# Kernel tuning notes

Hardware: AMD Instinct MI355X
Metric: run time of the kernel (lower is better)

Reference implementation:

```python
import jax, jax.numpy as jnp
import numpy as np

M0, M1, H = 128, 64, 8            # scalar mul, vector mul, num heads
AH0, AH1 = 16, 8                  # per-head irreps: 16x0e + 8x1e
D = M0 + 3 * M1                   # 320 node feature dim
DTP0 = M0 + M1                    # 192 scalar channels out of depthwise TP
DTP1 = M0 + 2 * M1                # 256 vector channels out of depthwise TP
WNUM = 2 * M0 + 3 * M1            # 448 TP path weights (uvu, edge mul=1)
RAD_IN, RAD_HID = 32, 64
N_NODES, N_EDGES = 10000, 160000
INV_SQRT3 = 1.0 / np.sqrt(3.0)    # CG norm for 1e x 1e -> 0e
INV_SQRT2 = 1.0 / np.sqrt(2.0)    # CG norm for 1e x 1e -> 1e


def _split(x, m0, m1):
    # e3nn layout: [m0 scalars | m1 vectors * 3 components]
    return x[..., :m0], x[..., m0:].reshape(x.shape[:-1] + (m1, 3))


def _silu(x):
    return x * jax.nn.sigmoid(x)


def _smooth_leaky(x, a=0.2):
    # SmoothLeakyReLU from equiformer
    return 0.5 * (1 + a) * x + 0.5 * (1 - a) * x * (2.0 * jax.nn.sigmoid(x) - 1.0)


def _dtp(s, v, e0, e1, w):
    # depthwise (uvu) tensor product of (M0x0e + M1x1e) with edge attr (1x0e + 1x1e)
    # s [E,M0], v [E,M1,3], e0 [E,1], e1 [E,3], w [E,WNUM] or [WNUM] (internal)
    w1, w2, w3, w4, w5 = jnp.split(w, [M0, 2 * M0, 2 * M0 + M1, 2 * M0 + 2 * M1], axis=-1)
    os1 = w1 * s * e0                                                  # 0e x 0e -> 0e
    os2 = w4 * (jnp.einsum('emc,ec->em', v, e1) * INV_SQRT3)           # 1e x 1e -> 0e
    ov1 = (w2 * s)[..., None] * e1[:, None, :]                         # 0e x 1e -> 1e
    ov2 = w3[..., None] * v * e0[..., None]                            # 1e x 0e -> 1e
    ov3 = w5[..., None] * (jnp.cross(v, e1[:, None, :]) * INV_SQRT2)   # 1e x 1e -> 1e
    return jnp.concatenate([os1, os2], -1), jnp.concatenate([ov1, ov2, ov3], -2)


def _forward(node_input, edge_src, edge_dst, edge_attr, edge_scalars,
             Wsrc_s, Wsrc_v, bsrc, Wdst_s, Wdst_v,
             rad_W1, rad_b1, rad_W2, rad_off,
             Wact_s, bact, Wact_v, Walpha, balpha, w_int,
             Wval_s, bval, Wval_v, alpha_dot, Wproj_s, bproj, Wproj_v):
    N = node_input.shape[0]
    E = edge_src.shape[0]
    s, v = _split(node_input, M0, M1)
    # merge_src / merge_dst: per-irrep linear (bias only on scalars of src)
    ms_s = s @ Wsrc_s + bsrc
    ms_v = jnp.einsum('nmc,mk->nkc', v, Wsrc_v)
    md_s = s @ Wdst_s
    md_v = jnp.einsum('nmc,mk->nkc', v, Wdst_v)
    msg_s = ms_s[edge_src] + md_s[edge_dst]          # [E, M0]
    msg_v = ms_v[edge_src] + md_v[edge_dst]          # [E, M1, 3]
    e0, e1 = edge_attr[:, :1], edge_attr[:, 1:4]
    # radial profile MLP -> edge-dependent TP weights
    w = _silu(edge_scalars @ rad_W1 + rad_b1) @ rad_W2 + rad_off       # [E, WNUM]
    ds, dv = _dtp(msg_s, msg_v, e0, e1, w)           # [E, DTP0], [E, DTP1, 3]
    # alpha branch: linear on TP scalars -> heads -> smooth leaky -> dot
    al = _smooth_leaky((ds @ Walpha + balpha).reshape(E, H, AH0))
    logits = jnp.einsum('ehk,hk->eh', al, alpha_dot[0])                # [E, H]
    # value branch: sep_act.lin + gate
    scal = ds @ Wact_s + bact                        # [E, M0+M1] scalars+gates
    gated_v = jnp.einsum('emc,mk->ekc', dv, Wact_v)  # [E, M1, 3]
    val_s = _silu(scal[:, :M0])
    val_v = gated_v * jax.nn.sigmoid(scal[:, M0:])[..., None]
    # sep_value: depthwise TP with internal weights + linear
    vs, vv = _dtp(val_s, val_v, e0, e1, w_int)
    out_s = vs @ Wval_s + bval                       # [E, H*AH0]
    out_v = jnp.einsum('emc,mk->ekc', vv, Wval_v)    # [E, H*AH1, 3]
    value = jnp.concatenate([out_s.reshape(E, H, AH0),
                             out_v.reshape(E, H, AH1 * 3)], axis=2)    # [E, H, 40]
    # softmax over incoming edges per destination node
    mx = jax.lax.stop_gradient(jax.ops.segment_max(logits, edge_dst, num_segments=N))
    mx = jnp.where(jnp.isfinite(mx), mx, 0.0)
    ex = jnp.exp(logits - mx[edge_dst])
    den = jax.ops.segment_sum(ex, edge_dst, num_segments=N)
    alpha = ex / (den[edge_dst] + 1e-16)             # [E, H]
    agg = jax.ops.segment_sum(value * alpha[..., None], edge_dst, num_segments=N)
    # heads2vec + output projection
    node_s = agg[:, :, :AH0].reshape(N, H * AH0)
    node_v = agg[:, :, AH0:].reshape(N, H * AH1, 3)
    po_s = node_s @ Wproj_s + bproj
    po_v = jnp.einsum('nmc,mk->nkc', node_v, Wproj_v)
    return jnp.concatenate([po_s, po_v.reshape(N, M1 * 3)], axis=1)


def _lin(key, fi, fo):
    return jax.random.normal(key, (fi, fo), jnp.float32) / np.sqrt(fi)


def setup_inputs() -> dict:
    ks = iter(jax.random.split(jax.random.key(0), 40))
    inp = {}
    inp['node_input'] = jax.random.normal(next(ks), (N_NODES, D), jnp.float32)
    inp['edge_src'] = jax.random.randint(next(ks), (N_EDGES,), 0, N_NODES)
    inp['edge_dst'] = jax.random.randint(next(ks), (N_EDGES,), 0, N_NODES)
    inp['edge_attr'] = jax.random.normal(next(ks), (N_EDGES, 4), jnp.float32)
    inp['edge_scalars'] = jax.random.normal(next(ks), (N_EDGES, RAD_IN), jnp.float32)
    inp['Wsrc_s'] = _lin(next(ks), M0, M0)
    inp['Wsrc_v'] = _lin(next(ks), M1, M1)
    inp['bsrc'] = 0.1 * jax.random.normal(next(ks), (M0,), jnp.float32)
    inp['Wdst_s'] = _lin(next(ks), M0, M0)
    inp['Wdst_v'] = _lin(next(ks), M1, M1)
    inp['rad_W1'] = _lin(next(ks), RAD_IN, RAD_HID)
    inp['rad_b1'] = 0.1 * jax.random.normal(next(ks), (RAD_HID,), jnp.float32)
    inp['rad_W2'] = _lin(next(ks), RAD_HID, WNUM)
    inp['rad_off'] = 0.1 * jax.random.normal(next(ks), (WNUM,), jnp.float32)
    inp['Wact_s'] = _lin(next(ks), DTP0, M0 + M1)
    inp['bact'] = 0.1 * jax.random.normal(next(ks), (M0 + M1,), jnp.float32)
    inp['Wact_v'] = _lin(next(ks), DTP1, M1)
    inp['Walpha'] = _lin(next(ks), DTP0, H * AH0)
    inp['balpha'] = 0.1 * jax.random.normal(next(ks), (H * AH0,), jnp.float32)
    inp['w_int'] = jax.random.normal(next(ks), (WNUM,), jnp.float32)
    inp['Wval_s'] = _lin(next(ks), DTP0, H * AH0)
    inp['bval'] = 0.1 * jax.random.normal(next(ks), (H * AH0,), jnp.float32)
    inp['Wval_v'] = _lin(next(ks), DTP1, H * AH1)
    inp['alpha_dot'] = jax.random.normal(next(ks), (1, H, AH0), jnp.float32) / np.sqrt(AH0)
    inp['Wproj_s'] = _lin(next(ks), H * AH0, M0)
    inp['bproj'] = 0.1 * jax.random.normal(next(ks), (M0,), jnp.float32)
    inp['Wproj_v'] = _lin(next(ks), H * AH1, M1)
    return inp


def reference(node_input, edge_src, edge_dst, edge_attr, edge_scalars,
              Wsrc_s, Wsrc_v, bsrc, Wdst_s, Wdst_v,
              rad_W1, rad_b1, rad_W2, rad_off,
              Wact_s, bact, Wact_v, Walpha, balpha, w_int,
              Wval_s, bval, Wval_v, alpha_dot, Wproj_s, bproj, Wproj_v):
    return _forward(node_input, edge_src, edge_dst, edge_attr, edge_scalars,
                    Wsrc_s, Wsrc_v, bsrc, Wdst_s, Wdst_v,
                    rad_W1, rad_b1, rad_W2, rad_off,
                    Wact_s, bact, Wact_v, Walpha, balpha, w_int,
                    Wval_s, bval, Wval_v, alpha_dot, Wproj_s, bproj, Wproj_v)
```

## Files before the change

kernel.cpp:

```cpp
#include <hip/hip_runtime.h>

#define NN 10000
#define NE 160000
#define INV_SQRT3f 0.57735026918962576f
#define INV_SQRT2f 0.70710678118654752f
#define VPLU 640000

typedef short bshort8 __attribute__((ext_vector_type(8)));
typedef float floatx4 __attribute__((ext_vector_type(4)));
#define MFMA16(a,b,c) __builtin_amdgcn_mfma_f32_16x16x32_bf16((a),(b),(c),0,0,0)

__device__ __forceinline__ float sigm(float x){ return 1.f/(1.f+__expf(-x)); }
__device__ __forceinline__ float siluf(float x){ return x*sigm(x); }
__device__ __forceinline__ float sleaky(float x){ return 0.6f*x + 0.4f*x*(2.f*sigm(x)-1.f); }
__device__ __forceinline__ unsigned short f2bf(float f){
  return (unsigned short)((__float_as_uint(f) + 0x8000u)>>16);
}
__device__ __forceinline__ float bf2f(unsigned short h){
  return __uint_as_float(((unsigned)h)<<16);
}
__device__ __forceinline__ unsigned cvtpk(float lo, float hi){
  unsigned r;
  asm("v_cvt_pk_bf16_f32 %0, %1, %2" : "=v"(r) : "v"(lo), "v"(hi));
  return r;
}
__device__ __forceinline__ float lo16f(unsigned u){ return __uint_as_float(u<<16); }
__device__ __forceinline__ float hi16f(unsigned u){ return __uint_as_float(u & 0xffff0000u); }

#define O_W1   0
#define O_W2   2048
#define O_WAS  30720
#define O_WAVT 67584
#define O_WAVB 75776
#define O_WVS  83968
#define O_WVVT 108544
#define O_WVVB 116736
#define O_WALP 124928
#define SWZ_TOTAL 149504

__global__ __launch_bounds__(256) void k_init(float* __restrict__ num,
                                              float* __restrict__ den,
                                              int* __restrict__ cnt) {
  int i = blockIdx.x*256 + threadIdx.x;
  if (i < NN*320) num[i] = 0.f;
  if (i < NN*8) den[i] = 0.f;
  if (i < NN) cnt[i] = 0;
}

__global__ __launch_bounds__(256) void k_hist(const int* __restrict__ edst,
                                              int* __restrict__ cnt) {
  int e = blockIdx.x*256 + threadIdx.x;
  if (e < NE) atomicAdd(&cnt[edst[e]], 1);
}

__global__ __launch_bounds__(256) void k_scan(const int* __restrict__ cnt,
                                              int* __restrict__ offs) {
  __shared__ int wsum[4];
  const int tid = threadIdx.x;
  const int lane = tid & 63, wave = tid >> 6;
  int v[40]; int s = 0;
  #pragma unroll
  for (int j=0;j<40;j++){ int i = tid*40+j; v[j] = (i<NN)?cnt[i]:0; s += v[j]; }
  int incl = s;
  #pragma unroll
  for (int d=1; d<64; d<<=1) { int t = __shfl_up(incl, d, 64); if (lane>=d) incl += t; }
  if (lane==63) wsum[wave] = incl;
  __syncthreads();
  int wbase = 0;
  for (int w=0; w<wave; ++w) wbase += wsum[w];
  int excl = wbase + incl - s;
  #pragma unroll
  for (int j=0;j<40;j++){ int i = tid*40+j; if (i<NN) offs[i] = excl; excl += v[j]; }
}

__global__ __launch_bounds__(256) void k_scatter(const int* __restrict__ edst,
                                                 int* __restrict__ offs,
                                                 int* __restrict__ perm) {
  int e = blockIdx.x*256 + threadIdx.x;
  if (e < NE) {
    int pos = atomicAdd(&offs[edst[e]], 1);
    perm[pos] = e;
  }
}

__global__ __launch_bounds__(256) void node_pre(
    const float* __restrict__ x,
    const float* __restrict__ Wsrc_s, const float* __restrict__ Wsrc_v,
    const float* __restrict__ bsrc,
    const float* __restrict__ Wdst_s, const float* __restrict__ Wdst_v,
    unsigned short* __restrict__ ms_s, unsigned short* __restrict__ md_s,
    unsigned short* __restrict__ ms_v, unsigned short* __restrict__ md_v) {
  __shared__ __align__(16) float s_s[128*8];
  __shared__ __align__(16) float s_v[192*8];
  const int tid = threadIdx.x;
  const int n0 = blockIdx.x*8;
  for (int idx = tid; idx < 8*320; idx += 256) {
    int n = idx/320, d = idx - n*320;
    float val = x[(n0+n)*320 + d];
    if (d < 128) s_s[d*8+n] = val;
    else         s_v[(d-128)*8+n] = val;
  }
  __syncthreads();
  {
    int g = tid>>7, j = tid&127;
    float accs[4], accd[4];
    float b = bsrc[j];
    #pragma unroll
    for (int i=0;i<4;i++){ accs[i]=b; accd[i]=0.f; }
    for (int k=0;k<128;k++) {
      float w1 = Wsrc_s[k*128+j], w2 = Wdst_s[k*128+j];
      float4 sv = *(const float4*)&s_s[k*8+g*4];
      accs[0]+=sv.x*w1; accs[1]+=sv.y*w1; accs[2]+=sv.z*w1; accs[3]+=sv.w*w1;
      accd[0]+=sv.x*w2; accd[1]+=sv.y*w2; accd[2]+=sv.z*w2; accd[3]+=sv.w*w2;
    }
    #pragma unroll
    for (int i=0;i<4;i++){ int n=n0+g*4+i; ms_s[n*128+j]=f2bf(accs[i]); md_s[n*128+j]=f2bf(accd[i]); }
  }
  if (tid < 192) {
    int c = tid>>6, k = tid&63;
    float accs[8], accd[8];
    #pragma unroll
    for (int e=0;e<8;e++){ accs[e]=0.f; accd[e]=0.f; }
    for (int m=0;m<64;m++) {
      float w1 = Wsrc_v[m*64+k], w2 = Wdst_v[m*64+k];
      float4 v0 = *(const float4*)&s_v[(m*3+c)*8];
      float4 v1 = *(const float4*)&s_v[(m*3+c)*8+4];
      accs[0]+=v0.x*w1; accs[1]+=v0.y*w1; accs[2]+=v0.z*w1; accs[3]+=v0.w*w1;
      accs[4]+=v1.x*w1; accs[5]+=v1.y*w1; accs[6]+=v1.z*w1; accs[7]+=v1.w*w1;
      accd[0]+=v0.x*w2; accd[1]+=v0.y*w2; accd[2]+=v0.z*w2; accd[3]+=v0.w*w2;
      accd[4]+=v1.x*w2; accd[5]+=v1.y*w2; accd[6]+=v1.z*w2; accd[7]+=v1.w*w2;
    }
    #pragma unroll
    for (int e=0;e<8;e++){
      int n=n0+e;
      ms_v[c*VPLU + n*64 + k] = f2bf(accs[e]);
      md_v[c*VPLU + n*64 + k] = f2bf(accd[e]);
    }
  }
}

__global__ __launch_bounds__(256) void k_prep(
    const float* __restrict__ W1, const float* __restrict__ W2,
    const float* __restrict__ WAs, const float* __restrict__ WAv,
    const float* __restrict__ WVs, const float* __restrict__ WVv,
    const float* __restrict__ WAl,
    unsigned short* __restrict__ swz) {
  int s = blockIdx.x*256 + threadIdx.x;
  if (s >= SWZ_TOTAL) return;
  const float* src; int base, N, KT, rowOff;
  if      (s < 2048)  { base=O_W1;   src=W1;  N=64;  KT=1; rowOff=0; }
  else if (s < 30720) { base=O_W2;   src=W2;  N=448; KT=2; rowOff=0; }
  else if (s < 67584) { base=O_WAS;  src=WAs; N=192; KT=6; rowOff=0; }
  else if (s < 75776) { base=O_WAVT; src=WAv; N=64;  KT=4; rowOff=0; }
  else if (s < 83968) { base=O_WAVB; src=WAv; N=64;  KT=4; rowOff=128; }
  else if (s < 108544){ base=O_WVS;  src=WVs; N=128; KT=6; rowOff=0; }
  else if (s < 116736){ base=O_WVVT; src=WVv; N=64;  KT=4; rowOff=0; }
  else if (s < 124928){ base=O_WVVB; src=WVv; N=64;  KT=4; rowOff=128; }
  else                { base=O_WALP; src=WAl; N=128; KT=6; rowOff=0; }
  int loc = s - base;
  int j = loc & 7, l = (loc>>3)&63, kt = (loc>>9)%KT, nt = loc/(512*KT);
  int row = kt*32 + (l>>4)*8 + j + rowOff;
  int col = nt*16 + (l&15);
  swz[s] = f2bf(src[row*N + col]);
}

__global__ __launch_bounds__(256, 5) void e_all(
    const unsigned short* __restrict__ ms_s, const unsigned short* __restrict__ md_s,
    const unsigned short* __restrict__ ms_v, const unsigned short* __restrict__ md_v,
    const int* __restrict__ esrc, const int* __restrict__ edst,
    const int* __restrict__ perm,
    const float* __restrict__ eattr, const float* __restrict__ escal,
    const float* __restrict__ rad_b1, const float* __restrict__ rad_off,
    const float* __restrict__ bact, const float* __restrict__ w_int,
    const float* __restrict__ bval,
    const float* __restrict__ balpha, const float* __restrict__ alpha_dot,
    const unsigned short* __restrict__ swz,
    float* __restrict__ den, float* __restrict__ num) {
  __shared__ __align__(16) char smem[30912];
  unsigned short* sw_v = (unsigned short*)smem;
  float* vout          = (float*)smem;
  unsigned short* ads  = (unsigned short*)(smem+6144);
  unsigned short* at1  = (unsigned short*)(smem+12544);
  unsigned short* advb = (unsigned short*)(smem+16896);
  unsigned short* aes  = (unsigned short*)(smem+16896);
  unsigned short* ah   = (unsigned short*)(smem+19456);
  float* s_e0 = (float*)(smem+29952);
  float* s_e1 = (float*)(smem+30016);
  float* s_ex = (float*)(smem+30208);
  int* s_eid  = (int*)(smem+30720);
  int* s_src  = (int*)(smem+30784);
  int* s_dst  = (int*)(smem+30848);
  const int tid  = threadIdx.x;
  const int lane = tid & 63, wave = tid >> 6;
  const int quad = lane >> 4, l15 = lane & 15;
  const int bswz = (blockIdx.x & 7)*1250 + (blockIdx.x >> 3);
  const int eb = bswz*16;

  if (tid < 16) {
    int eid = perm[eb+tid];
    s_eid[tid] = eid; s_src[tid] = esrc[eid]; s_dst[tid] = edst[eid];
  }
  __syncthreads();
  if (tid >= 64 && tid < 128) {
    int t = tid-64, e = t>>2, q = t&3;
    float a = eattr[s_eid[e]*4+q];
    if (q == 0) s_e0[e] = a; else s_e1[(q-1)*16+e] = a;
  }
  {
    int e = tid>>4, i0 = (tid&15)*2;
    float2 es = *(const float2*)&escal[s_eid[e]*32+i0];
    *(unsigned*)&aes[e*40+i0] = cvtpk(es.x, es.y);
  }
  __syncthreads();

  {
    int nt = wave, col = nt*16 + l15;
    bshort8 a = *(const bshort8*)&aes[l15*40 + quad*8];
    bshort8 b = *(const bshort8*)&swz[O_W1 + (nt*64 + lane)*8];
    float bb = rad_b1[col];
    floatx4 acc = {bb,bb,bb,bb};
    acc = MFMA16(a, b, acc);
    #pragma unroll
    for (int r=0;r<4;r++) ah[(quad*4+r)*72 + col] = f2bf(siluf(acc[r]));
  }
  __syncthreads();

  {
    bshort8 ha0 = *(const bshort8*)&ah[l15*72 + quad*8];
    bshort8 ha1 = *(const bshort8*)&ah[l15*72 + 32 + quad*8];
    int src_[4], dst_[4];
    #pragma unroll
    for (int r=0;r<4;r++){ int e=quad*4+r; src_[r]=s_src[e]; dst_[r]=s_dst[e]; }
    #pragma unroll
    for (int p=0;p<2;p++) {
      int nt1 = wave*2+p, nt2 = nt1+8;
      int m = nt1*16 + l15;
      float o1 = rad_off[m], o2 = rad_off[128+m];
      floatx4 a1 = {o1,o1,o1,o1}, a2 = {o2,o2,o2,o2};
      a1 = MFMA16(ha0, *(const bshort8*)&swz[O_W2 + ((nt1*2+0)*64+lane)*8], a1);
      a1 = MFMA16(ha1, *(const bshort8*)&swz[O_W2 + ((nt1*2+1)*64+lane)*8], a1);
      a2 = MFMA16(ha0, *(const bshort8*)&swz[O_W2 + ((nt2*2+0)*64+lane)*8], a2);
      a2 = MFMA16(ha1, *(const bshort8*)&swz[O_W2 + ((nt2*2+1)*64+lane)*8], a2);
      #pragma unroll
      for (int r=0;r<4;r++) {
        int e = quad*4+r;
        float msgs = bf2f(ms_s[src_[r]*128+m]) + bf2f(md_s[dst_[r]*128+m]);
        ads[e*200+m] = f2bf(a1[r]*msgs*s_e0[e]);
        at1[e*136+m] = f2bf(a2[r]*msgs);
      }
    }
    #pragma unroll
    for (int q=0;q<3;q++) {
      int nt = 16 + wave*3 + q, col = nt*16 + l15;
      float o = rad_off[col];
      floatx4 acc = {o,o,o,o};
      acc = MFMA16(ha0, *(const bshort8*)&swz[O_W2 + ((nt*2+0)*64+lane)*8], acc);
      acc = MFMA16(ha1, *(const bshort8*)&swz[O_W2 + ((nt*2+1)*64+lane)*8], acc);
      #pragma unroll
      for (int r=0;r<4;r++) sw_v[(quad*4+r)*192 + (col-256)] = f2bf(acc[r]);
    }
  }
  __syncthreads();

  #pragma unroll
  for (int it = 0; it < 2; ++it) {
    int t = tid + it*256;
    int e = t>>5, pr = t&31;
    int k0 = pr*2;
    int sb = s_src[e]*64 + k0, db = s_dst[e]*64 + k0;
    unsigned usx = *(const unsigned*)&ms_v[0*VPLU+sb];
    unsigned usy = *(const unsigned*)&ms_v[1*VPLU+sb];
    unsigned usz = *(const unsigned*)&ms_v[2*VPLU+sb];
    unsigned udx = *(const unsigned*)&md_v[0*VPLU+db];
    unsigned udy = *(const unsigned*)&md_v[1*VPLU+db];
    unsigned udz = *(const unsigned*)&md_v[2*VPLU+db];
    unsigned uw3 = *(const unsigned*)&sw_v[e*192 + k0];
    unsigned uw4 = *(const unsigned*)&sw_v[e*192 + 64 + k0];
    unsigned uw5 = *(const unsigned*)&sw_v[e*192 + 128 + k0];
    float ex1 = s_e1[0+e], ey1 = s_e1[16+e], ez1 = s_e1[32+e];
    float e0 = s_e0[e];
    float vx0 = lo16f(usx)+lo16f(udx), vx1 = hi16f(usx)+hi16f(udx);
    float vy0 = lo16f(usy)+lo16f(udy), vy1 = hi16f(usy)+hi16f(udy);
    float vz0 = lo16f(usz)+lo16f(udz), vz1 = hi16f(usz)+hi16f(udz);
    float d0 = vx0*ex1 + vy0*ey1 + vz0*ez1;
    float d1 = vx1*ex1 + vy1*ey1 + vz1*ez1;
    *(unsigned*)&ads[e*200+128+k0] =
        cvtpk(lo16f(uw4)*d0*INV_SQRT3f, hi16f(uw4)*d1*INV_SQRT3f);
    float w30 = lo16f(uw3)*e0, w31 = hi16f(uw3)*e0;
    float w50 = lo16f(uw5)*INV_SQRT2f, w51 = hi16f(uw5)*INV_SQRT2f;
    *(unsigned*)&advb[0*2176 + e*136 + k0] = cvtpk(w30*vx0, w31*vx1);
    *(unsigned*)&advb[1*2176 + e*136 + k0] = cvtpk(w30*vy0, w31*vy1);
    *(unsigned*)&advb[2*2176 + e*136 + k0] = cvtpk(w30*vz0, w31*vz1);
    *(unsigned*)&advb[0*2176 + e*136 + 64+k0] =
        cvtpk(w50*(vy0*ez1 - vz0*ey1), w51*(vy1*ez1 - vz1*ey1));
    *(unsigned*)&advb[1*2176 + e*136 + 64+k0] =
        cvtpk(w50*(vz0*ex1 - vx0*ez1), w51*(vz1*ex1 - vx1*ez1));
    *(unsigned*)&advb[2*2176 + e*136 + 64+k0] =
        cvtpk(w50*(vx0*ey1 - vy0*ex1), w51*(vx1*ey1 - vy1*ex1));
  }
  __syncthreads();

  floatx4 sc0, sc1, sc2, gsa, gb0, gb1, gb2;
  {
    bshort8 fa[6];
    #pragma unroll
    for (int kt=0;kt<6;kt++) fa[kt] = *(const bshort8*)&ads[l15*200 + kt*32 + quad*8];
    #pragma unroll
    for (int t=0;t<2;t++) {
      int h = wave*2 + t;
      int col = h*16 + l15;
      float bb = balpha[col];
      floatx4 acc = {bb,bb,bb,bb};
      #pragma unroll
      for (int kt=0;kt<6;kt++)
        acc = MFMA16(fa[kt], *(const bshort8*)&swz[O_WALP + ((h*6+kt)*64+lane)*8], acc);
      float ad = alpha_dot[col];
      float exv[4];
      #pragma unroll
      for (int r=0;r<4;r++) {
        float p = sleaky(acc[r])*ad;
        p += __shfl_xor(p, 1);
        p += __shfl_xor(p, 2);
        p += __shfl_xor(p, 4);
        p += __shfl_xor(p, 8);
        float ex = __expf(p);
        exv[r] = ex;
        if (l15 == 0) s_ex[(quad*4+r)*8+h] = ex;
      }
      if (l15 == 0) {
        float racc = exv[0]; int cur = s_dst[quad*4];
        #pragma unroll
        for (int r=1;r<4;r++) {
          int d = s_dst[quad*4+r];
          if (d != cur) { atomicAdd(&den[cur*8+h], racc); racc = 0.f; cur = d; }
          racc += exv[r];
        }
        atomicAdd(&den[cur*8+h], racc);
      }
    }
    {
      float bb = bact[wave*16 + l15];
      floatx4 a0 = {bb,bb,bb,bb};
      #pragma unroll
      for (int kt=0;kt<6;kt++)
        a0 = MFMA16(fa[kt], *(const bshort8*)&swz[O_WAS + ((wave*6+kt)*64+lane)*8], a0);
      sc0 = a0;
    }
    {
      float bb = bact[(wave+4)*16 + l15];
      floatx4 a1 = {bb,bb,bb,bb};
      #pragma unroll
      for (int kt=0;kt<6;kt++)
        a1 = MFMA16(fa[kt], *(const bshort8*)&swz[O_WAS + (((wave+4)*6+kt)*64+lane)*8], a1);
      sc1 = a1;
    }
    {
      float bb = bact[(wave+8)*16 + l15];
      floatx4 a2 = {bb,bb,bb,bb};
      #pragma unroll
      for (int kt=0;kt<6;kt++)
        a2 = MFMA16(fa[kt], *(const bshort8*)&swz[O_WAS + (((wave+8)*6+kt)*64+lane)*8], a2);
      sc2 = a2;
    }
    bshort8 ft[4];
    #pragma unroll
    for (int kt=0;kt<4;kt++) ft[kt] = *(const bshort8*)&at1[l15*136 + kt*32 + quad*8];
    {
      floatx4 acc = {0.f,0.f,0.f,0.f};
      #pragma unroll
      for (int kt=0;kt<4;kt++)
        acc = MFMA16(ft[kt], *(const bshort8*)&swz[O_WAVT + ((wave*4+kt)*64+lane)*8], acc);
      gsa = acc;
    }
    #pragma unroll
    for (int c=0;c<3;c++) {
      floatx4 acc = {0.f,0.f,0.f,0.f};
      #pragma unroll
      for (int kt=0;kt<4;kt++) {
        bshort8 fb = *(const bshort8*)&advb[c*2176 + l15*136 + kt*32 + quad*8];
        acc = MFMA16(fb, *(const bshort8*)&swz[O_WAVB + ((wave*4+kt)*64+lane)*8], acc);
      }
      if (c==0) gb0 = acc; else if (c==1) gb1 = acc; else gb2 = acc;
    }
  }
  __syncthreads();

  {
    const int k = wave*16 + l15;
    #pragma unroll
    for (int r=0;r<4;r++) {
      int row = quad*4 + r;
      float e0 = s_e0[row];
      {
        float v = siluf(sc0[r]);
        ads[row*200+k] = f2bf(w_int[k]*v*e0);
        at1[row*136+k] = f2bf(w_int[128+k]*v);
      }
      {
        int m = 64+k;
        float v = siluf(sc1[r]);
        ads[row*200+m] = f2bf(w_int[m]*v*e0);
        at1[row*136+m] = f2bf(w_int[128+m]*v);
      }
      {
        float sg = sigm(sc2[r]);
        float gs = gsa[r];
        float ex1 = s_e1[0+row], ey1 = s_e1[16+row], ez1 = s_e1[32+row];
        float v0 = (gs*ex1 + gb0[r])*sg;
        float v1 = (gs*ey1 + gb1[r])*sg;
        float v2 = (gs*ez1 + gb2[r])*sg;
        float d = v0*ex1 + v1*ey1 + v2*ez1;
        ads[row*200+128+k] = f2bf(w_int[320+k]*d*INV_SQRT3f);
        float w3v = w_int[256+k]*e0;
        float w5  = w_int[384+k]*INV_SQRT2f;
        advb[0*2176 + row*136 + k] = f2bf(w3v*v0);
        advb[1*2176 + row*136 + k] = f2bf(w3v*v1);
        advb[2*2176 + row*136 + k] = f2bf(w3v*v2);
        advb[0*2176 + row*136 + 64+k] = f2bf(w5*(v1*ez1 - v2*ey1));
        advb[1*2176 + row*136 + 64+k] = f2bf(w5*(v2*ex1 - v0*ez1));
        advb[2*2176 + row*136 + 64+k] = f2bf(w5*(v0*ey1 - v1*ex1));
      }
    }
  }
  __syncthreads();

  {
    bshort8 fa[6];
    #pragma unroll
    for (int kt=0;kt<6;kt++) fa[kt] = *(const bshort8*)&ads[l15*200 + kt*32 + quad*8];
    __syncthreads();
    #pragma unroll
    for (int t=0;t<2;t++) {
      int h = wave + 4*t;
      float bb = bval[h*16 + l15];
      floatx4 acc = {bb,bb,bb,bb};
      #pragma unroll
      for (int kt=0;kt<6;kt++)
        acc = MFMA16(fa[kt], *(const bshort8*)&swz[O_WVS + ((h*6+kt)*64+lane)*8], acc);
      #pragma unroll
      for (int r=0;r<4;r++) {
        int row = quad*4 + r;
        vout[row*132 + h*16 + l15] = acc[r]*s_ex[row*8+h];
      }
    }
  }
  __syncthreads();

  if (tid < 128) {
    const int j = tid, h = j>>4, jj = j&15;
    float acc = 0.f; int cur = s_dst[0];
    #pragma unroll
    for (int e = 0; e < 16; ++e) {
      int d = s_dst[e];
      if (d != cur) { atomicAdd(&num[cur*320 + h*40 + jj], acc); acc = 0.f; cur = d; }
      acc += vout[e*132 + j];
    }
    atomicAdd(&num[cur*320 + h*40 + jj], acc);
  }
  __syncthreads();

  {
    bshort8 ft[4];
    #pragma unroll
    for (int kt=0;kt<4;kt++) ft[kt] = *(const bshort8*)&at1[l15*136 + kt*32 + quad*8];
    floatx4 vsh = {0.f,0.f,0.f,0.f};
    #pragma unroll
    for (int kt=0;kt<4;kt++)
      vsh = MFMA16(ft[kt], *(const bshort8*)&swz[O_WVVT + ((wave*4+kt)*64+lane)*8], vsh);
    const int k = wave*16 + l15;
    const int h = k>>3, q = k&7;
    #pragma unroll
    for (int c=0;c<3;c++) {
      floatx4 acc = {0.f,0.f,0.f,0.f};
      #pragma unroll
      for (int kt=0;kt<4;kt++) {
        bshort8 fb = *(const bshort8*)&advb[c*2176 + l15*136 + kt*32 + quad*8];
        acc = MFMA16(fb, *(const bshort8*)&swz[O_WVVB + ((wave*4+kt)*64+lane)*8], acc);
      }
      #pragma unroll
      for (int r=0;r<4;r++) {
        int row = quad*4 + r;
        vout[row*194 + h*24 + q*3 + c] =
            (acc[r] + s_e1[c*16+row]*vsh[r]) * s_ex[row*8+h];
      }
    }
  }
  __syncthreads();

  if (tid < 192) {
    const int jj = tid;
    const int h = jj/24, rr = jj - h*24;
    float acc = 0.f; int cur = s_dst[0];
    #pragma unroll
    for (int e = 0; e < 16; ++e) {
      int d = s_dst[e];
      if (d != cur) { atomicAdd(&num[cur*320 + h*40 + 16 + rr], acc); acc = 0.f; cur = d; }
      acc += vout[e*194 + jj];
    }
    atomicAdd(&num[cur*320 + h*40 + 16 + rr], acc);
  }
}

__global__ __launch_bounds__(256) void node_post(
    const float* __restrict__ num, const float* __restrict__ den,
    const float* __restrict__ Wproj_s, const float* __restrict__ bproj,
    const float* __restrict__ Wproj_v, float* __restrict__ out) {
  __shared__ __align__(16) float s_ns[128*8];
  __shared__ __align__(16) float s_nv[192*8];
  const int tid = threadIdx.x;
  const int n0 = blockIdx.x*8;
  for (int idx = tid; idx < 8*320; idx += 256) {
    int n = idx/320, j = idx - n*320;
    int h = j/40, r = j - h*40;
    float a = num[(n0+n)*320+j] / (den[(n0+n)*8+h] + 1e-16f);
    if (r < 16) s_ns[(h*16+r)*8+n] = a;
    else        s_nv[(h*24 + (r-16))*8+n] = a;
  }
  __syncthreads();
  {
    int g = tid>>7, j = tid&127;
    float acc[4]; float b = bproj[j];
    #pragma unroll
    for (int i=0;i<4;i++) acc[i]=b;
    for (int k=0;k<128;k++) {
      float wv = Wproj_s[k*128+j];
      float4 s4 = *(const float4*)&s_ns[k*8+g*4];
      acc[0]+=s4.x*wv; acc[1]+=s4.y*wv; acc[2]+=s4.z*wv; acc[3]+=s4.w*wv;
    }
    #pragma unroll
    for (int i=0;i<4;i++) out[(n0+g*4+i)*320 + j] = acc[i];
  }
  if (tid < 192) {
    int c = tid>>6, k = tid&63;
    float acc[8];
    #pragma unroll
    for (int e=0;e<8;e++) acc[e]=0.f;
    for (int m=0;m<64;m++) {
      float wv = Wproj_v[m*64+k];
      float4 v0 = *(const float4*)&s_nv[(m*3+c)*8];
      float4 v1 = *(const float4*)&s_nv[(m*3+c)*8+4];
      acc[0]+=v0.x*wv; acc[1]+=v0.y*wv; acc[2]+=v0.z*wv; acc[3]+=v0.w*wv;
      acc[4]+=v1.x*wv; acc[5]+=v1.y*wv; acc[6]+=v1.z*wv; acc[7]+=v1.w*wv;
    }
    #pragma unroll
    for (int e=0;e<8;e++) out[(n0+e)*320 + 128 + k*3 + c] = acc[e];
  }
}

extern "C" void kernel_launch(void* const* d_in, const int* in_sizes, int n_in,
                              void* d_out, int out_size, void* d_ws, size_t ws_size,
                              hipStream_t stream) {
  (void)in_sizes; (void)n_in; (void)out_size; (void)ws_size;
  const float* node_input = (const float*)d_in[0];
  const int*   esrc       = (const int*)d_in[1];
  const int*   edst       = (const int*)d_in[2];
  const float* eattr      = (const float*)d_in[3];
  const float* escal      = (const float*)d_in[4];
  const float* Wsrc_s     = (const float*)d_in[5];
  const float* Wsrc_v     = (const float*)d_in[6];
  const float* bsrc       = (const float*)d_in[7];
  const float* Wdst_s     = (const float*)d_in[8];
  const float* Wdst_v     = (const float*)d_in[9];
  const float* rad_W1     = (const float*)d_in[10];
  const float* rad_b1     = (const float*)d_in[11];
  const float* rad_W2     = (const float*)d_in[12];
  const float* rad_off    = (const float*)d_in[13];
  const float* Wact_s     = (const float*)d_in[14];
  const float* bact       = (const float*)d_in[15];
  const float* Wact_v     = (const float*)d_in[16];
  const float* Walpha     = (const float*)d_in[17];
  const float* balpha     = (const float*)d_in[18];
  const float* w_int      = (const float*)d_in[19];
  const float* Wval_s     = (const float*)d_in[20];
  const float* bval       = (const float*)d_in[21];
  const float* Wval_v     = (const float*)d_in[22];
  const float* alpha_dot  = (const float*)d_in[23];
  const float* Wproj_s    = (const float*)d_in[24];
  const float* bproj      = (const float*)d_in[25];
  const float* Wproj_v    = (const float*)d_in[26];
  float* out = (float*)d_out;

  char* wsb = (char*)d_ws;
  unsigned short* ms_s16 = (unsigned short*)(wsb);
  unsigned short* md_s16 = (unsigned short*)(wsb + 2560000);
  unsigned short* ms_v16 = (unsigned short*)(wsb + 5120000);
  unsigned short* md_v16 = (unsigned short*)(wsb + 8960000);
  float* den             = (float*)(wsb + 12800000);
  float* num             = (float*)(wsb + 13120000);
  unsigned short* swz    = (unsigned short*)(wsb + 25920000);
  int* cnt  = (int*)(wsb + 26220032);
  int* offs = (int*)(wsb + 26260032);
  int* perm = (int*)(wsb + 26300032);

  k_prep<<<584, 256, 0, stream>>>(rad_W1, rad_W2, Wact_s, Wact_v, Wval_s, Wval_v, Walpha, swz);
  k_init<<<12500, 256, 0, stream>>>(num, den, cnt);
  k_hist<<<625, 256, 0, stream>>>(edst, cnt);
  k_scan<<<1, 256, 0, stream>>>(cnt, offs);
  k_scatter<<<625, 256, 0, stream>>>(edst, offs, perm);
  node_pre<<<1250, 256, 0, stream>>>(node_input, Wsrc_s, Wsrc_v, bsrc, Wdst_s, Wdst_v,
                                     ms_s16, md_s16, ms_v16, md_v16);
  e_all<<<10000, 256, 0, stream>>>(ms_s16, md_s16, ms_v16, md_v16, esrc, edst, perm, eattr, escal,
                                   rad_b1, rad_off, bact, w_int, bval,
                                   balpha, alpha_dot, swz, den, num);
  node_post<<<1250, 256, 0, stream>>>(num, den, Wproj_s, bproj, Wproj_v, out);
}
```

Before: 387.3 us.

## Fold internal TP weights into value weights, merge prep kernels, shrink edge LDS

```diff
diff --git a/kernel.cpp b/kernel.cpp
--- a/kernel.cpp
+++ b/kernel.cpp
@@ -24,8 +24,6 @@
   asm("v_cvt_pk_bf16_f32 %0, %1, %2" : "=v"(r) : "v"(lo), "v"(hi));
   return r;
 }
-__device__ __forceinline__ float lo16f(unsigned u){ return __uint_as_float(u<<16); }
-__device__ __forceinline__ float hi16f(unsigned u){ return __uint_as_float(u & 0xffff0000u); }
 
 #define O_W1   0
 #define O_W2   2048
@@ -38,13 +36,99 @@
 #define O_WALP 124928
 #define SWZ_TOTAL 149504
 
-__global__ __launch_bounds__(256) void k_init(float* __restrict__ num,
-                                              float* __restrict__ den,
-                                              int* __restrict__ cnt) {
-  int i = blockIdx.x*256 + threadIdx.x;
-  if (i < NN*320) num[i] = 0.f;
-  if (i < NN*8) den[i] = 0.f;
-  if (i < NN) cnt[i] = 0;
+__global__ __launch_bounds__(256) void k_pre_all(
+    const float* __restrict__ x,
+    const float* __restrict__ Wsrc_s, const float* __restrict__ Wsrc_v,
+    const float* __restrict__ bsrc,
+    const float* __restrict__ Wdst_s, const float* __restrict__ Wdst_v,
+    unsigned short* __restrict__ ms_s, unsigned short* __restrict__ md_s,
+    unsigned short* __restrict__ ms_v, unsigned short* __restrict__ md_v,
+    const float* __restrict__ W1, const float* __restrict__ W2,
+    const float* __restrict__ WAs, const float* __restrict__ WAv,
+    const float* __restrict__ WVs, const float* __restrict__ WVv,
+    const float* __restrict__ WAl, const float* __restrict__ w_int,
+    unsigned short* __restrict__ swz,
+    float* __restrict__ num, float* __restrict__ den, int* __restrict__ cnt) {
+  __shared__ __align__(16) float s_s[128*8];
+  __shared__ __align__(16) float s_v[192*8];
+  const int tid = threadIdx.x;
+  const int b = blockIdx.x;
+  if (b >= 1834) {
+    int base = (b-1834)*256 + tid;
+    float4 z = {0.f,0.f,0.f,0.f};
+    for (int i = base; i < 800000; i += 554496) ((float4*)num)[i] = z;
+    if (base < 20000) ((float4*)den)[base] = z;
+    if (base < 10000) cnt[base] = 0;
+    return;
+  }
+  if (b >= 1250) {
+    int s = (b-1250)*256 + tid;
+    if (s >= SWZ_TOTAL) return;
+    const float* src; int base, N, KT, rowOff;
+    if      (s < 2048)  { base=O_W1;   src=W1;  N=64;  KT=1; rowOff=0; }
+    else if (s < 30720) { base=O_W2;   src=W2;  N=448; KT=2; rowOff=0; }
+    else if (s < 67584) { base=O_WAS;  src=WAs; N=192; KT=6; rowOff=0; }
+    else if (s < 75776) { base=O_WAVT; src=WAv; N=64;  KT=4; rowOff=0; }
+    else if (s < 83968) { base=O_WAVB; src=WAv; N=64;  KT=4; rowOff=128; }
+    else if (s < 108544){ base=O_WVS;  src=WVs; N=128; KT=6; rowOff=0; }
+    else if (s < 116736){ base=O_WVVT; src=WVv; N=64;  KT=4; rowOff=0; }
+    else if (s < 124928){ base=O_WVVB; src=WVv; N=64;  KT=4; rowOff=128; }
+    else                { base=O_WALP; src=WAl; N=128; KT=6; rowOff=0; }
+    int loc = s - base;
+    int j = loc & 7, l = (loc>>3)&63, kt = (loc>>9)%KT, nt = loc/(512*KT);
+    int row = kt*32 + (l>>4)*8 + j + rowOff;
+    int col = nt*16 + (l&15);
+    float scl = 1.f;
+    if      (base == O_WVS)  scl = (row < 128) ? w_int[row] : w_int[192+row]*INV_SQRT3f;
+    else if (base == O_WVVT) scl = w_int[128+row];
+    else if (base == O_WVVB) scl = (row < 192) ? w_int[128+row] : w_int[192+row]*INV_SQRT2f;
+    swz[s] = f2bf(src[row*N + col] * scl);
+    return;
+  }
+  const int n0 = b*8;
+  for (int idx = tid; idx < 8*320; idx += 256) {
+    int n = idx/320, d = idx - n*320;
+    float val = x[(n0+n)*320 + d];
+    if (d < 128) s_s[d*8+n] = val;
+    else         s_v[(d-128)*8+n] = val;
+  }
+  __syncthreads();
+  {
+    int g = tid>>7, j = tid&127;
+    float accs[4], accd[4];
+    float bb = bsrc[j];
+    #pragma unroll
+    for (int i=0;i<4;i++){ accs[i]=bb; accd[i]=0.f; }
+    for (int k=0;k<128;k++) {
+      float w1 = Wsrc_s[k*128+j], w2 = Wdst_s[k*128+j];
+      float4 sv = *(const float4*)&s_s[k*8+g*4];
+      accs[0]+=sv.x*w1; accs[1]+=sv.y*w1; accs[2]+=sv.z*w1; accs[3]+=sv.w*w1;
+      accd[0]+=sv.x*w2; accd[1]+=sv.y*w2; accd[2]+=sv.z*w2; accd[3]+=sv.w*w2;
+    }
+    #pragma unroll
+    for (int i=0;i<4;i++){ int n=n0+g*4+i; ms_s[n*128+j]=f2bf(accs[i]); md_s[n*128+j]=f2bf(accd[i]); }
+  }
+  if (tid < 192) {
+    int c = tid>>6, k = tid&63;
+    float accs[8], accd[8];
+    #pragma unroll
+    for (int e=0;e<8;e++){ accs[e]=0.f; accd[e]=0.f; }
+    for (int m=0;m<64;m++) {
+      float w1 = Wsrc_v[m*64+k], w2 = Wdst_v[m*64+k];
+      float4 v0 = *(const float4*)&s_v[(m*3+c)*8];
+      float4 v1 = *(const float4*)&s_v[(m*3+c)*8+4];
+      accs[0]+=v0.x*w1; accs[1]+=v0.y*w1; accs[2]+=v0.z*w1; accs[3]+=v0.w*w1;
+      accs[4]+=v1.x*w1; accs[5]+=v1.y*w1; accs[6]+=v1.z*w1; accs[7]+=v1.w*w1;
+      accd[0]+=v0.x*w2; accd[1]+=v0.y*w2; accd[2]+=v0.z*w2; accd[3]+=v0.w*w2;
+      accd[4]+=v1.x*w2; accd[5]+=v1.y*w2; accd[6]+=v1.z*w2; accd[7]+=v1.w*w2;
+    }
+    #pragma unroll
+    for (int e=0;e<8;e++){
+      int n=n0+e;
+      ms_v[c*VPLU + n*64 + k] = f2bf(accs[e]);
+      md_v[c*VPLU + n*64 + k] = f2bf(accd[e]);
+    }
+  }
 }
 
 __global__ __launch_bounds__(256) void k_hist(const int* __restrict__ edst,
@@ -83,113 +167,31 @@
   }
 }
 
-__global__ __launch_bounds__(256) void node_pre(
-    const float* __restrict__ x,
-    const float* __restrict__ Wsrc_s, const float* __restrict__ Wsrc_v,
-    const float* __restrict__ bsrc,
-    const float* __restrict__ Wdst_s, const float* __restrict__ Wdst_v,
-    unsigned short* __restrict__ ms_s, unsigned short* __restrict__ md_s,
-    unsigned short* __restrict__ ms_v, unsigned short* __restrict__ md_v) {
-  __shared__ __align__(16) float s_s[128*8];
-  __shared__ __align__(16) float s_v[192*8];
-  const int tid = threadIdx.x;
-  const int n0 = blockIdx.x*8;
-  for (int idx = tid; idx < 8*320; idx += 256) {
-    int n = idx/320, d = idx - n*320;
-    float val = x[(n0+n)*320 + d];
-    if (d < 128) s_s[d*8+n] = val;
-    else         s_v[(d-128)*8+n] = val;
-  }
-  __syncthreads();
-  {
-    int g = tid>>7, j = tid&127;
-    float accs[4], accd[4];
-    float b = bsrc[j];
-    #pragma unroll
-    for (int i=0;i<4;i++){ accs[i]=b; accd[i]=0.f; }
-    for (int k=0;k<128;k++) {
-      float w1 = Wsrc_s[k*128+j], w2 = Wdst_s[k*128+j];
-      float4 sv = *(const float4*)&s_s[k*8+g*4];
-      accs[0]+=sv.x*w1; accs[1]+=sv.y*w1; accs[2]+=sv.z*w1; accs[3]+=sv.w*w1;
-      accd[0]+=sv.x*w2; accd[1]+=sv.y*w2; accd[2]+=sv.z*w2; accd[3]+=sv.w*w2;
-    }
-    #pragma unroll
-    for (int i=0;i<4;i++){ int n=n0+g*4+i; ms_s[n*128+j]=f2bf(accs[i]); md_s[n*128+j]=f2bf(accd[i]); }
-  }
-  if (tid < 192) {
-    int c = tid>>6, k = tid&63;
-    float accs[8], accd[8];
-    #pragma unroll
-    for (int e=0;e<8;e++){ accs[e]=0.f; accd[e]=0.f; }
-    for (int m=0;m<64;m++) {
-      float w1 = Wsrc_v[m*64+k], w2 = Wdst_v[m*64+k];
-      float4 v0 = *(const float4*)&s_v[(m*3+c)*8];
-      float4 v1 = *(const float4*)&s_v[(m*3+c)*8+4];
-      accs[0]+=v0.x*w1; accs[1]+=v0.y*w1; accs[2]+=v0.z*w1; accs[3]+=v0.w*w1;
-      accs[4]+=v1.x*w1; accs[5]+=v1.y*w1; accs[6]+=v1.z*w1; accs[7]+=v1.w*w1;
-      accd[0]+=v0.x*w2; accd[1]+=v0.y*w2; accd[2]+=v0.z*w2; accd[3]+=v0.w*w2;
-      accd[4]+=v1.x*w2; accd[5]+=v1.y*w2; accd[6]+=v1.z*w2; accd[7]+=v1.w*w2;
-    }
-    #pragma unroll
-    for (int e=0;e<8;e++){
-      int n=n0+e;
-      ms_v[c*VPLU + n*64 + k] = f2bf(accs[e]);
-      md_v[c*VPLU + n*64 + k] = f2bf(accd[e]);
-    }
-  }
-}
-
-__global__ __launch_bounds__(256) void k_prep(
-    const float* __restrict__ W1, const float* __restrict__ W2,
-    const float* __restrict__ WAs, const float* __restrict__ WAv,
-    const float* __restrict__ WVs, const float* __restrict__ WVv,
-    const float* __restrict__ WAl,
-    unsigned short* __restrict__ swz) {
-  int s = blockIdx.x*256 + threadIdx.x;
-  if (s >= SWZ_TOTAL) return;
-  const float* src; int base, N, KT, rowOff;
-  if      (s < 2048)  { base=O_W1;   src=W1;  N=64;  KT=1; rowOff=0; }
-  else if (s < 30720) { base=O_W2;   src=W2;  N=448; KT=2; rowOff=0; }
-  else if (s < 67584) { base=O_WAS;  src=WAs; N=192; KT=6; rowOff=0; }
-  else if (s < 75776) { base=O_WAVT; src=WAv; N=64;  KT=4; rowOff=0; }
-  else if (s < 83968) { base=O_WAVB; src=WAv; N=64;  KT=4; rowOff=128; }
-  else if (s < 108544){ base=O_WVS;  src=WVs; N=128; KT=6; rowOff=0; }
-  else if (s < 116736){ base=O_WVVT; src=WVv; N=64;  KT=4; rowOff=0; }
-  else if (s < 124928){ base=O_WVVB; src=WVv; N=64;  KT=4; rowOff=128; }
-  else                { base=O_WALP; src=WAl; N=128; KT=6; rowOff=0; }
-  int loc = s - base;
-  int j = loc & 7, l = (loc>>3)&63, kt = (loc>>9)%KT, nt = loc/(512*KT);
-  int row = kt*32 + (l>>4)*8 + j + rowOff;
-  int col = nt*16 + (l&15);
-  swz[s] = f2bf(src[row*N + col]);
-}
-
-__global__ __launch_bounds__(256, 5) void e_all(
+__global__ __launch_bounds__(256, 6) void e_all(
     const unsigned short* __restrict__ ms_s, const unsigned short* __restrict__ md_s,
     const unsigned short* __restrict__ ms_v, const unsigned short* __restrict__ md_v,
     const int* __restrict__ esrc, const int* __restrict__ edst,
     const int* __restrict__ perm,
     const float* __restrict__ eattr, const float* __restrict__ escal,
     const float* __restrict__ rad_b1, const float* __restrict__ rad_off,
-    const float* __restrict__ bact, const float* __restrict__ w_int,
+    const float* __restrict__ bact,
     const float* __restrict__ bval,
     const float* __restrict__ balpha, const float* __restrict__ alpha_dot,
     const unsigned short* __restrict__ swz,
     float* __restrict__ den, float* __restrict__ num) {
-  __shared__ __align__(16) char smem[30912];
-  unsigned short* sw_v = (unsigned short*)smem;
-  float* vout          = (float*)smem;
-  unsigned short* ads  = (unsigned short*)(smem+6144);
-  unsigned short* at1  = (unsigned short*)(smem+12544);
-  unsigned short* advb = (unsigned short*)(smem+16896);
-  unsigned short* aes  = (unsigned short*)(smem+16896);
-  unsigned short* ah   = (unsigned short*)(smem+19456);
-  float* s_e0 = (float*)(smem+29952);
-  float* s_e1 = (float*)(smem+30016);
-  float* s_ex = (float*)(smem+30208);
-  int* s_eid  = (int*)(smem+30720);
-  int* s_src  = (int*)(smem+30784);
-  int* s_dst  = (int*)(smem+30848);
+  __shared__ __align__(16) char smem[24768];
+  unsigned short* ads  = (unsigned short*)smem;
+  unsigned short* at1  = (unsigned short*)(smem+6400);
+  unsigned short* advb = (unsigned short*)(smem+10752);
+  unsigned short* aes  = (unsigned short*)(smem+10752);
+  unsigned short* ah   = (unsigned short*)(smem+12032);
+  float* vout          = (float*)(smem+10752);
+  float* s_e0 = (float*)(smem+23808);
+  float* s_e1 = (float*)(smem+23872);
+  float* s_ex = (float*)(smem+24064);
+  int* s_eid  = (int*)(smem+24576);
+  int* s_src  = (int*)(smem+24640);
+  int* s_dst  = (int*)(smem+24704);
   const int tid  = threadIdx.x;
   const int lane = tid & 63, wave = tid >> 6;
   const int quad = lane >> 4, l15 = lane & 15;
@@ -228,6 +230,7 @@
   {
     bshort8 ha0 = *(const bshort8*)&ah[l15*72 + quad*8];
     bshort8 ha1 = *(const bshort8*)&ah[l15*72 + 32 + quad*8];
+    __syncthreads();
     int src_[4], dst_[4];
     #pragma unroll
     for (int r=0;r<4;r++){ int e=quad*4+r; src_[r]=s_src[e]; dst_[r]=s_dst[e]; }
@@ -249,54 +252,49 @@
         at1[e*136+m] = f2bf(a2[r]*msgs);
       }
     }
-    #pragma unroll
-    for (int q=0;q<3;q++) {
-      int nt = 16 + wave*3 + q, col = nt*16 + l15;
-      float o = rad_off[col];
+    floatx4 aw3, aw4, aw5;
+    {
+      int nt = 16 + wave; float o = rad_off[nt*16+l15];
       floatx4 acc = {o,o,o,o};
       acc = MFMA16(ha0, *(const bshort8*)&swz[O_W2 + ((nt*2+0)*64+lane)*8], acc);
       acc = MFMA16(ha1, *(const bshort8*)&swz[O_W2 + ((nt*2+1)*64+lane)*8], acc);
-      #pragma unroll
-      for (int r=0;r<4;r++) sw_v[(quad*4+r)*192 + (col-256)] = f2bf(acc[r]);
-    }
-  }
-  __syncthreads();
-
-  #pragma unroll
-  for (int it = 0; it < 2; ++it) {
-    int t = tid + it*256;
-    int e = t>>5, pr = t&31;
-    int k0 = pr*2;
-    int sb = s_src[e]*64 + k0, db = s_dst[e]*64 + k0;
-    unsigned usx = *(const unsigned*)&ms_v[0*VPLU+sb];
-    unsigned usy = *(const unsigned*)&ms_v[1*VPLU+sb];
-    unsigned usz = *(const unsigned*)&ms_v[2*VPLU+sb];
-    unsigned udx = *(const unsigned*)&md_v[0*VPLU+db];
-    unsigned udy = *(const unsigned*)&md_v[1*VPLU+db];
-    unsigned udz = *(const unsigned*)&md_v[2*VPLU+db];
-    unsigned uw3 = *(const unsigned*)&sw_v[e*192 + k0];
-    unsigned uw4 = *(const unsigned*)&sw_v[e*192 + 64 + k0];
-    unsigned uw5 = *(const unsigned*)&sw_v[e*192 + 128 + k0];
-    float ex1 = s_e1[0+e], ey1 = s_e1[16+e], ez1 = s_e1[32+e];
-    float e0 = s_e0[e];
-    float vx0 = lo16f(usx)+lo16f(udx), vx1 = hi16f(usx)+hi16f(udx);
-    float vy0 = lo16f(usy)+lo16f(udy), vy1 = hi16f(usy)+hi16f(udy);
-    float vz0 = lo16f(usz)+lo16f(udz), vz1 = hi16f(usz)+hi16f(udz);
-    float d0 = vx0*ex1 + vy0*ey1 + vz0*ez1;
-    float d1 = vx1*ex1 + vy1*ey1 + vz1*ez1;
-    *(unsigned*)&ads[e*200+128+k0] =
-        cvtpk(lo16f(uw4)*d0*INV_SQRT3f, hi16f(uw4)*d1*INV_SQRT3f);
-    float w30 = lo16f(uw3)*e0, w31 = hi16f(uw3)*e0;
-    float w50 = lo16f(uw5)*INV_SQRT2f, w51 = hi16f(uw5)*INV_SQRT2f;
-    *(unsigned*)&advb[0*2176 + e*136 + k0] = cvtpk(w30*vx0, w31*vx1);
-    *(unsigned*)&advb[1*2176 + e*136 + k0] = cvtpk(w30*vy0, w31*vy1);
-    *(unsigned*)&advb[2*2176 + e*136 + k0] = cvtpk(w30*vz0, w31*vz1);
-    *(unsigned*)&advb[0*2176 + e*136 + 64+k0] =
-        cvtpk(w50*(vy0*ez1 - vz0*ey1), w51*(vy1*ez1 - vz1*ey1));
-    *(unsigned*)&advb[1*2176 + e*136 + 64+k0] =
-        cvtpk(w50*(vz0*ex1 - vx0*ez1), w51*(vz1*ex1 - vx1*ez1));
-    *(unsigned*)&advb[2*2176 + e*136 + 64+k0] =
-        cvtpk(w50*(vx0*ey1 - vy0*ex1), w51*(vx1*ey1 - vy1*ex1));
+      aw3 = acc;
+    }
+    {
+      int nt = 20 + wave; float o = rad_off[nt*16+l15];
+      floatx4 acc = {o,o,o,o};
+      acc = MFMA16(ha0, *(const bshort8*)&swz[O_W2 + ((nt*2+0)*64+lane)*8], acc);
+      acc = MFMA16(ha1, *(const bshort8*)&swz[O_W2 + ((nt*2+1)*64+lane)*8], acc);
+      aw4 = acc;
+    }
+    {
+      int nt = 24 + wave; float o = rad_off[nt*16+l15];
+      floatx4 acc = {o,o,o,o};
+      acc = MFMA16(ha0, *(const bshort8*)&swz[O_W2 + ((nt*2+0)*64+lane)*8], acc);
+      acc = MFMA16(ha1, *(const bshort8*)&swz[O_W2 + ((nt*2+1)*64+lane)*8], acc);
+      aw5 = acc;
+    }
+    const int k = wave*16 + l15;
+    #pragma unroll
+    for (int r=0;r<4;r++) {
+      int e = quad*4 + r;
+      int sb = src_[r]*64 + k, db = dst_[r]*64 + k;
+      float vx = bf2f(ms_v[0*VPLU+sb]) + bf2f(md_v[0*VPLU+db]);
+      float vy = bf2f(ms_v[1*VPLU+sb]) + bf2f(md_v[1*VPLU+db]);
+      float vz = bf2f(ms_v[2*VPLU+sb]) + bf2f(md_v[2*VPLU+db]);
+      float ex1 = s_e1[0+e], ey1 = s_e1[16+e], ez1 = s_e1[32+e];
+      float e0 = s_e0[e];
+      float d = vx*ex1 + vy*ey1 + vz*ez1;
+      ads[e*200+128+k] = f2bf(aw4[r]*d*INV_SQRT3f);
+      float w3v = aw3[r]*e0;
+      float w5  = aw5[r]*INV_SQRT2f;
+      advb[0*2176 + e*136 + k] = f2bf(w3v*vx);
+      advb[1*2176 + e*136 + k] = f2bf(w3v*vy);
+      advb[2*2176 + e*136 + k] = f2bf(w3v*vz);
+      advb[0*2176 + e*136 + 64+k] = f2bf(w5*(vy*ez1 - vz*ey1));
+      advb[1*2176 + e*136 + 64+k] = f2bf(w5*(vz*ex1 - vx*ez1));
+      advb[2*2176 + e*136 + 64+k] = f2bf(w5*(vx*ey1 - vy*ex1));
+    }
   }
   __syncthreads();
 
@@ -393,14 +391,13 @@
       float e0 = s_e0[row];
       {
         float v = siluf(sc0[r]);
-        ads[row*200+k] = f2bf(w_int[k]*v*e0);
-        at1[row*136+k] = f2bf(w_int[128+k]*v);
+        ads[row*200+k] = f2bf(v*e0);
+        at1[row*136+k] = f2bf(v);
       }
       {
-        int m = 64+k;
         float v = siluf(sc1[r]);
-        ads[row*200+m] = f2bf(w_int[m]*v*e0);
-        at1[row*136+m] = f2bf(w_int[128+m]*v);
+        ads[row*200+64+k] = f2bf(v*e0);
+        at1[row*136+64+k] = f2bf(v);
       }
       {
         float sg = sigm(sc2[r]);
@@ -410,17 +407,62 @@
         float v1 = (gs*ey1 + gb1[r])*sg;
         float v2 = (gs*ez1 + gb2[r])*sg;
         float d = v0*ex1 + v1*ey1 + v2*ez1;
-        ads[row*200+128+k] = f2bf(w_int[320+k]*d*INV_SQRT3f);
-        float w3v = w_int[256+k]*e0;
-        float w5  = w_int[384+k]*INV_SQRT2f;
-        advb[0*2176 + row*136 + k] = f2bf(w3v*v0);
-        advb[1*2176 + row*136 + k] = f2bf(w3v*v1);
-        advb[2*2176 + row*136 + k] = f2bf(w3v*v2);
-        advb[0*2176 + row*136 + 64+k] = f2bf(w5*(v1*ez1 - v2*ey1));
-        advb[1*2176 + row*136 + 64+k] = f2bf(w5*(v2*ex1 - v0*ez1));
-        advb[2*2176 + row*136 + 64+k] = f2bf(w5*(v0*ey1 - v1*ex1));
-      }
-    }
+        ads[row*200+128+k] = f2bf(d);
+        advb[0*2176 + row*136 + k] = f2bf(v0*e0);
+        advb[1*2176 + row*136 + k] = f2bf(v1*e0);
+        advb[2*2176 + row*136 + k] = f2bf(v2*e0);
+        advb[0*2176 + row*136 + 64+k] = f2bf(v1*ez1 - v2*ey1);
+        advb[1*2176 + row*136 + 64+k] = f2bf(v2*ex1 - v0*ez1);
+        advb[2*2176 + row*136 + 64+k] = f2bf(v0*ey1 - v1*ex1);
+      }
+    }
+  }
+  __syncthreads();
+
+  {
+    bshort8 ft[4];
+    #pragma unroll
+    for (int kt=0;kt<4;kt++) ft[kt] = *(const bshort8*)&at1[l15*136 + kt*32 + quad*8];
+    floatx4 vsh = {0.f,0.f,0.f,0.f};
+    #pragma unroll
+    for (int kt=0;kt<4;kt++)
+      vsh = MFMA16(ft[kt], *(const bshort8*)&swz[O_WVVT + ((wave*4+kt)*64+lane)*8], vsh);
+    floatx4 vb0, vb1, vb2;
+    #pragma unroll
+    for (int c=0;c<3;c++) {
+      floatx4 acc = {0.f,0.f,0.f,0.f};
+      #pragma unroll
+      for (int kt=0;kt<4;kt++) {
+        bshort8 fb = *(const bshort8*)&advb[c*2176 + l15*136 + kt*32 + quad*8];
+        acc = MFMA16(fb, *(const bshort8*)&swz[O_WVVB + ((wave*4+kt)*64+lane)*8], acc);
+      }
+      if (c==0) vb0 = acc; else if (c==1) vb1 = acc; else vb2 = acc;
+    }
+    __syncthreads();
+    const int k = wave*16 + l15;
+    const int h = k>>3, q = k&7;
+    #pragma unroll
+    for (int r=0;r<4;r++) {
+      int row = quad*4 + r;
+      float exr = s_ex[row*8+h];
+      vout[row*194 + h*24 + q*3 + 0] = (vb0[r] + s_e1[0*16+row]*vsh[r])*exr;
+      vout[row*194 + h*24 + q*3 + 1] = (vb1[r] + s_e1[1*16+row]*vsh[r])*exr;
+      vout[row*194 + h*24 + q*3 + 2] = (vb2[r] + s_e1[2*16+row]*vsh[r])*exr;
+    }
+  }
+  __syncthreads();
+
+  if (tid < 192) {
+    const int jj = tid;
+    const int h = jj/24, rr = jj - h*24;
+    float acc = 0.f; int cur = s_dst[0];
+    #pragma unroll
+    for (int e = 0; e < 16; ++e) {
+      int d = s_dst[e];
+      if (d != cur) { atomicAdd(&num[cur*320 + h*40 + 16 + rr], acc); acc = 0.f; cur = d; }
+      acc += vout[e*194 + jj];
+    }
+    atomicAdd(&num[cur*320 + h*40 + 16 + rr], acc);
   }
   __syncthreads();
 
@@ -428,7 +470,6 @@
     bshort8 fa[6];
     #pragma unroll
     for (int kt=0;kt<6;kt++) fa[kt] = *(const bshort8*)&ads[l15*200 + kt*32 + quad*8];
-    __syncthreads();
     #pragma unroll
     for (int t=0;t<2;t++) {
       int h = wave + 4*t;
@@ -456,48 +497,6 @@
       acc += vout[e*132 + j];
     }
     atomicAdd(&num[cur*320 + h*40 + jj], acc);
-  }
-  __syncthreads();
-
-  {
-    bshort8 ft[4];
-    #pragma unroll
-    for (int kt=0;kt<4;kt++) ft[kt] = *(const bshort8*)&at1[l15*136 + kt*32 + quad*8];
-    floatx4 vsh = {0.f,0.f,0.f,0.f};
-    #pragma unroll
-    for (int kt=0;kt<4;kt++)
-      vsh = MFMA16(ft[kt], *(const bshort8*)&swz[O_WVVT + ((wave*4+kt)*64+lane)*8], vsh);
-    const int k = wave*16 + l15;
-    const int h = k>>3, q = k&7;
-    #pragma unroll
-    for (int c=0;c<3;c++) {
-      floatx4 acc = {0.f,0.f,0.f,0.f};
-      #pragma unroll
-      for (int kt=0;kt<4;kt++) {
-        bshort8 fb = *(const bshort8*)&advb[c*2176 + l15*136 + kt*32 + quad*8];
-        acc = MFMA16(fb, *(const bshort8*)&swz[O_WVVB + ((wave*4+kt)*64+lane)*8], acc);
-      }
-      #pragma unroll
-      for (int r=0;r<4;r++) {
-        int row = quad*4 + r;
-        vout[row*194 + h*24 + q*3 + c] =
-            (acc[r] + s_e1[c*16+row]*vsh[r]) * s_ex[row*8+h];
-      }
-    }
-  }
-  __syncthreads();
-
-  if (tid < 192) {
-    const int jj = tid;
-    const int h = jj/24, rr = jj - h*24;
-    float acc = 0.f; int cur = s_dst[0];
-    #pragma unroll
-    for (int e = 0; e < 16; ++e) {
-      int d = s_dst[e];
-      if (d != cur) { atomicAdd(&num[cur*320 + h*40 + 16 + rr], acc); acc = 0.f; cur = d; }
-      acc += vout[e*194 + jj];
-    }
-    atomicAdd(&num[cur*320 + h*40 + 16 + rr], acc);
   }
 }
 
@@ -592,15 +591,15 @@
   int* offs = (int*)(wsb + 26260032);
   int* perm = (int*)(wsb + 26300032);
 
-  k_prep<<<584, 256, 0, stream>>>(rad_W1, rad_W2, Wact_s, Wact_v, Wval_s, Wval_v, Walpha, swz);
-  k_init<<<12500, 256, 0, stream>>>(num, den, cnt);
+  k_pre_all<<<4000, 256, 0, stream>>>(node_input, Wsrc_s, Wsrc_v, bsrc, Wdst_s, Wdst_v,
+                                      ms_s16, md_s16, ms_v16, md_v16,
+                                      rad_W1, rad_W2, Wact_s, Wact_v, Wval_s, Wval_v,
+                                      Walpha, w_int, swz, num, den, cnt);
   k_hist<<<625, 256, 0, stream>>>(edst, cnt);
   k_scan<<<1, 256, 0, stream>>>(cnt, offs);
   k_scatter<<<625, 256, 0, stream>>>(edst, offs, perm);
-  node_pre<<<1250, 256, 0, stream>>>(node_input, Wsrc_s, Wsrc_v, bsrc, Wdst_s, Wdst_v,
-                                     ms_s16, md_s16, ms_v16, md_v16);
   e_all<<<10000, 256, 0, stream>>>(ms_s16, md_s16, ms_v16, md_v16, esrc, edst, perm, eattr, escal,
-                                   rad_b1, rad_off, bact, w_int, bval,
+                                   rad_b1, rad_off, bact, bval,
                                    balpha, alpha_dot, swz, den, num);
   node_post<<<1250, 256, 0, stream>>>(num, den, Wproj_s, bproj, Wproj_v, out);
 }
```

Result: no change. 383.4 us (-1.0%).
